# Performance work log

Hardware: AMD Instinct MI355X
Metric: run time of the kernel (lower is better)

## Reference

```python
import jax, jax.numpy as jnp
import numpy as np

B, S, V = 2, 2048, 50257
MIN_TOKENS_RATIO = 0.25
WARMUP_STEPS = 1000
THRESHOLD_SENSITIVITY = 0.5


def setup_inputs() -> dict:
    key = jax.random.key(0)
    k1, k2 = jax.random.split(key)
    logits = jax.random.normal(k1, (B, S, V), dtype=jnp.float32)
    targets = jax.random.randint(k2, (B, S), 0, V, dtype=jnp.int64)
    return {"logits": logits, "targets": targets, "step_count": 1000}


def _forward(logits, targets, step_count):
    vocab = logits.shape[-1]
    lf = logits.reshape(-1, vocab)          # (N, V)
    tf = targets.reshape(-1)                # (N,)
    n_tokens = lf.shape[0]

    # Single fused log-softmax pass shared by CE loss and difficulty scoring.
    logp = jax.nn.log_softmax(lf, axis=-1)  # (N, V)
    per_token_loss = -jnp.take_along_axis(logp, tf[:, None], axis=1)[:, 0]  # (N,)

    # --- difficulty scoring (no-grad in original: stop_gradient) ---
    logp_sg = jax.lax.stop_gradient(logp)
    p = jnp.exp(logp_sg)
    entropy = -jnp.sum(p * logp_sg, axis=-1)            # (N,)
    log_v = jnp.log(jnp.asarray(vocab, jnp.float32))
    ent_norm = entropy / log_v
    top2, _ = jax.lax.top_k(p, 2)                        # (N, 2)
    confidence = top2[:, 0]
    margin = top2[:, 0] - top2[:, 1]
    loss_norm = jax.lax.stop_gradient(per_token_loss) / log_v
    # 'combined' scoring: mean of normalized entropy, (1-margin), normalized loss
    difficulty = (ent_norm + (1.0 - margin) + loss_norm) / 3.0

    # --- warmup schedule + dynamic threshold ---
    progress = jnp.minimum(1.0, jnp.asarray(step_count, jnp.float32) / max(1, WARMUP_STEPS))
    base_ratio = 1.0 - progress * (1.0 - MIN_TOKENS_RATIO)
    mean_conf = jnp.mean(confidence)
    ratio = jnp.clip(base_ratio * (1.0 + THRESHOLD_SENSITIVITY * (0.5 - mean_conf)), 0.05, 1.0)

    # --- top-k selection via threshold on sorted difficulty (jit-safe dynamic k) ---
    k = jnp.clip(jnp.round(ratio * n_tokens).astype(jnp.int32), 1, n_tokens)
    sorted_desc = jnp.sort(difficulty)[::-1]
    thresh = jnp.take(sorted_desc, k - 1)
    mask = (difficulty >= thresh).astype(per_token_loss.dtype)  # (N,)

    tokens_selected = jnp.sum(mask)
    loss = jnp.sum(per_token_loss * mask) / jnp.maximum(tokens_selected, 1.0)
    return loss


def reference(logits, targets, step_count):
    return _forward(logits, targets, step_count)
```

## Files before the change

kernel.cpp:

```cpp
#include <hip/hip_runtime.h>

#define VOCAB 50257
#define NTOK 4096
#define P1_THREADS 256
#define P2_THREADS 1024
#define NEG_HUGE -3.402823466e+38f

struct OS { float m1, m2, Z, S1; };

__device__ __forceinline__ void os_init(OS& s) {
  s.m1 = NEG_HUGE; s.m2 = NEG_HUGE; s.Z = 0.0f; s.S1 = 0.0f;
}

__device__ __forceinline__ void os_update(OS& s, float x) {
  float nm1 = fmaxf(s.m1, x);
  float d   = s.m1 - nm1;
  float dx  = x - nm1;
  float ed  = __expf(d);
  float edx = __expf(dx);
  s.m2 = fmaxf(s.m2, fminf(s.m1, x));
  s.S1 = fmaf(dx, edx, ed * fmaf(d, s.Z, s.S1));
  s.Z  = fmaf(ed, s.Z, edx);
  s.m1 = nm1;
}

__device__ __forceinline__ void os_merge(OS& a, const OS& b) {
  float M   = fmaxf(a.m1, b.m1);
  float m2  = fmaxf(fmaxf(a.m2, b.m2), fminf(a.m1, b.m1));
  float ea  = __expf(a.m1 - M);
  float eb  = __expf(b.m1 - M);
  float S1  = ea * fmaf(a.m1 - M, a.Z, a.S1) + eb * fmaf(b.m1 - M, b.Z, b.S1);
  float Z   = fmaf(ea, a.Z, eb * b.Z);
  a.m1 = M; a.m2 = m2; a.Z = Z; a.S1 = S1;
}

__global__ __launch_bounds__(P1_THREADS) void cggr_rowstats(
    const float* __restrict__ logits, const int* __restrict__ targets,
    float* __restrict__ diff, float* __restrict__ loss, float* __restrict__ conf)
{
  const int row = blockIdx.x;
  const float* __restrict__ x = logits + (size_t)row * VOCAB;
  const int tid = threadIdx.x;

  float xt = 0.0f;
  if (tid == 0) {
    int t = targets[row];
    xt = x[t];
  }

  OS s0, s1, s2, s3;
  os_init(s0); os_init(s1); os_init(s2); os_init(s3);

  const int head = (4 - (row & 3)) & 3;
  const int nv4  = (VOCAB - head) >> 2;
  const float4* __restrict__ x4 = (const float4*)(x + head);

  for (int i = tid; i < nv4; i += P1_THREADS) {
    float4 v = x4[i];
    os_update(s0, v.x);
    os_update(s1, v.y);
    os_update(s2, v.z);
    os_update(s3, v.w);
  }
  if (tid < head) os_update(s0, x[tid]);
  for (int i = head + 4 * nv4 + tid; i < VOCAB; i += P1_THREADS) os_update(s1, x[i]);

  os_merge(s0, s1); os_merge(s2, s3); os_merge(s0, s2);

  for (int m = 1; m < 64; m <<= 1) {
    OS o;
    o.m1 = __shfl_xor(s0.m1, m);
    o.m2 = __shfl_xor(s0.m2, m);
    o.Z  = __shfl_xor(s0.Z,  m);
    o.S1 = __shfl_xor(s0.S1, m);
    os_merge(s0, o);
  }

  __shared__ OS sred[P1_THREADS / 64];
  const int lane = tid & 63, wid = tid >> 6;
  if (lane == 0) sred[wid] = s0;
  __syncthreads();

  if (tid == 0) {
    OS a = sred[0];
    for (int w = 1; w < P1_THREADS / 64; ++w) os_merge(a, sred[w]);
    float m       = a.m1;
    float lnZ     = logf(a.Z);
    float ptl     = m + lnZ - xt;
    float entropy = lnZ - a.S1 / a.Z;
    float log_v   = logf((float)VOCAB);
    float cf      = 1.0f / a.Z;
    float margin  = (1.0f - __expf(a.m2 - m)) / a.Z;
    float dif     = (entropy / log_v + (1.0f - margin) + ptl / log_v) / 3.0f;
    diff[row] = dif;
    loss[row] = ptl;
    conf[row] = cf;
  }
}

__global__ __launch_bounds__(P2_THREADS) void cggr_finalize(
    const float* __restrict__ diff, const float* __restrict__ loss,
    const float* __restrict__ conf, const int* __restrict__ step_ptr,
    float* __restrict__ out)
{
  __shared__ float s[NTOK];
  __shared__ float rl[P2_THREADS / 64];
  __shared__ float rc[P2_THREADS / 64];
  __shared__ int ks;

  const int tid  = threadIdx.x;
  const int lane = tid & 63, wid = tid >> 6;

  float c = 0.0f;
  for (int i = tid; i < NTOK; i += P2_THREADS) c += conf[i];
  for (int m = 1; m < 64; m <<= 1) c += __shfl_xor(c, m);
  if (lane == 0) rl[wid] = c;
  __syncthreads();

  if (tid == 0) {
    float sum = 0.0f;
    for (int w = 0; w < P2_THREADS / 64; ++w) sum += rl[w];
    float mean_conf  = sum / (float)NTOK;
    float step       = (float)step_ptr[0];
    float progress   = fminf(1.0f, step / 1000.0f);
    float base_ratio = 1.0f - progress * (1.0f - 0.25f);
    float ratio      = base_ratio * (1.0f + 0.5f * (0.5f - mean_conf));
    ratio = fminf(fmaxf(ratio, 0.05f), 1.0f);
    int k = (int)rintf(ratio * (float)NTOK);
    k = k < 1 ? 1 : (k > NTOK ? NTOK : k);
    ks = k;
  }

  for (int i = tid; i < NTOK; i += P2_THREADS) s[i] = diff[i];
  __syncthreads();

  for (int size = 2; size <= NTOK; size <<= 1) {
    for (int stride = size >> 1; stride > 0; stride >>= 1) {
      for (int t = tid; t < NTOK / 2; t += P2_THREADS) {
        int i = 2 * t - (t & (stride - 1));
        int j = i + stride;
        bool up = ((i & size) == 0);
        float a = s[i], b = s[j];
        if ((a > b) == up) { s[i] = b; s[j] = a; }
      }
      __syncthreads();
    }
  }

  const float thresh = s[NTOK - ks];

  float ls = 0.0f, cnt = 0.0f;
  for (int i = tid; i < NTOK; i += P2_THREADS) {
    float d = diff[i];
    if (d >= thresh) { ls += loss[i]; cnt += 1.0f; }
  }
  for (int m = 1; m < 64; m <<= 1) {
    ls  += __shfl_xor(ls, m);
    cnt += __shfl_xor(cnt, m);
  }
  if (lane == 0) { rl[wid] = ls; rc[wid] = cnt; }
  __syncthreads();
  if (tid == 0) {
    float tl = 0.0f, tc = 0.0f;
    for (int w = 0; w < P2_THREADS / 64; ++w) { tl += rl[w]; tc += rc[w]; }
    out[0] = tl / fmaxf(tc, 1.0f);
  }
}

extern "C" void kernel_launch(void* const* d_in, const int* in_sizes, int n_in,
                              void* d_out, int out_size, void* d_ws, size_t ws_size,
                              hipStream_t stream) {
  const float* logits  = (const float*)d_in[0];
  const int*   targets = (const int*)d_in[1];
  const int*   step    = (const int*)d_in[2];
  float* ws   = (float*)d_ws;
  float* diff = ws;
  float* loss = ws + NTOK;
  float* conf = ws + 2 * NTOK;

  hipLaunchKernelGGL(cggr_rowstats, dim3(NTOK), dim3(P1_THREADS), 0, stream,
                     logits, targets, diff, loss, conf);
  hipLaunchKernelGGL(cggr_finalize, dim3(1), dim3(P2_THREADS), 0, stream,
                     diff, loss, conf, step, (float*)d_out);
}
```

Measured before the change: 188.3 us.

## Batch online-softmax updates per float4 and replace bitonic sort with radix select

The row-stats kernel now reduces each float4 locally (max, second max, four exps) and merges once into the running state. That cuts the per-element rescale exponentials from two to roughly one plus a quarter, and the merge uses a single exp via a select. The finalize kernel drops the full 4096-element bitonic sort in shared memory. It finds the k-th largest difficulty with a 32-step bitwise radix select on order-preserving integer keys, using wave-level counts and a double-buffered shared reduction. The second kernel is a single block, so this mainly shortens its serial tail, while the first kernel is limited by memory bandwidth.

```diff
diff --git a/kernel.cpp b/kernel.cpp
--- a/kernel.cpp
+++ b/kernel.cpp
@@ -6,32 +6,35 @@
 #define P2_THREADS 1024
 #define NEG_HUGE -3.402823466e+38f
 
-struct OS { float m1, m2, Z, S1; };
+struct OS { float m, m2, Z, S1; };
 
 __device__ __forceinline__ void os_init(OS& s) {
-  s.m1 = NEG_HUGE; s.m2 = NEG_HUGE; s.Z = 0.0f; s.S1 = 0.0f;
+  s.m = NEG_HUGE; s.m2 = NEG_HUGE; s.Z = 0.0f; s.S1 = 0.0f;
 }
 
-__device__ __forceinline__ void os_update(OS& s, float x) {
-  float nm1 = fmaxf(s.m1, x);
-  float d   = s.m1 - nm1;
-  float dx  = x - nm1;
-  float ed  = __expf(d);
-  float edx = __expf(dx);
-  s.m2 = fmaxf(s.m2, fminf(s.m1, x));
-  s.S1 = fmaf(dx, edx, ed * fmaf(d, s.Z, s.S1));
-  s.Z  = fmaf(ed, s.Z, edx);
-  s.m1 = nm1;
+__device__ __forceinline__ void os_merge(OS& a, float ml, float m2l, float zl, float s1l) {
+  float M  = fmaxf(a.m, ml);
+  float mn = fminf(a.m, ml);
+  float m2 = fmaxf(fmaxf(a.m2, m2l), mn);
+  float e  = __expf(mn - M);
+  bool  om = a.m >= ml;
+  float eo = om ? 1.0f : e;
+  float en = om ? e : 1.0f;
+  float S1 = eo * fmaf(a.m - M, a.Z, a.S1) + en * fmaf(ml - M, zl, s1l);
+  float Z  = fmaf(eo, a.Z, en * zl);
+  a.m = M; a.m2 = m2; a.Z = Z; a.S1 = S1;
 }
 
-__device__ __forceinline__ void os_merge(OS& a, const OS& b) {
-  float M   = fmaxf(a.m1, b.m1);
-  float m2  = fmaxf(fmaxf(a.m2, b.m2), fminf(a.m1, b.m1));
-  float ea  = __expf(a.m1 - M);
-  float eb  = __expf(b.m1 - M);
-  float S1  = ea * fmaf(a.m1 - M, a.Z, a.S1) + eb * fmaf(b.m1 - M, b.Z, b.S1);
-  float Z   = fmaf(ea, a.Z, eb * b.Z);
-  a.m1 = M; a.m2 = m2; a.Z = Z; a.S1 = S1;
+__device__ __forceinline__ void os_update4(OS& s, float4 v) {
+  float a  = fmaxf(v.x, v.y), b = fminf(v.x, v.y);
+  float c  = fmaxf(v.z, v.w), d = fminf(v.z, v.w);
+  float ml  = fmaxf(a, c);
+  float m2l = fmaxf(fminf(a, c), fmaxf(b, d));
+  float d0 = v.x - ml, d1 = v.y - ml, d2 = v.z - ml, d3 = v.w - ml;
+  float e0 = __expf(d0), e1 = __expf(d1), e2 = __expf(d2), e3 = __expf(d3);
+  float zl  = (e0 + e1) + (e2 + e3);
+  float s1l = fmaf(d0, e0, fmaf(d1, e1, fmaf(d2, e2, d3 * e3)));
+  os_merge(s, ml, m2l, zl, s1l);
 }
 
 __global__ __launch_bounds__(P1_THREADS) void cggr_rowstats(
@@ -43,37 +46,36 @@
   const int tid = threadIdx.x;
 
   float xt = 0.0f;
-  if (tid == 0) {
-    int t = targets[row];
-    xt = x[t];
-  }
-
-  OS s0, s1, s2, s3;
-  os_init(s0); os_init(s1); os_init(s2); os_init(s3);
+  if (tid == 0) xt = x[targets[row]];
 
   const int head = (4 - (row & 3)) & 3;
   const int nv4  = (VOCAB - head) >> 2;
   const float4* __restrict__ x4 = (const float4*)(x + head);
 
-  for (int i = tid; i < nv4; i += P1_THREADS) {
-    float4 v = x4[i];
-    os_update(s0, v.x);
-    os_update(s1, v.y);
-    os_update(s2, v.z);
-    os_update(s3, v.w);
+  OS s0, s1; os_init(s0); os_init(s1);
+
+  int i = tid;
+  for (; i + P1_THREADS < nv4; i += 2 * P1_THREADS) {
+    float4 va = x4[i];
+    float4 vb = x4[i + P1_THREADS];
+    os_update4(s0, va);
+    os_update4(s1, vb);
   }
-  if (tid < head) os_update(s0, x[tid]);
-  for (int i = head + 4 * nv4 + tid; i < VOCAB; i += P1_THREADS) os_update(s1, x[i]);
+  if (i < nv4) os_update4(s0, x4[i]);
 
-  os_merge(s0, s1); os_merge(s2, s3); os_merge(s0, s2);
+  if (tid < head) os_merge(s1, x[tid], NEG_HUGE, 1.0f, 0.0f);
+  for (int t = head + 4 * nv4 + tid; t < VOCAB; t += P1_THREADS)
+    os_merge(s1, x[t], NEG_HUGE, 1.0f, 0.0f);
+
+  os_merge(s0, s1.m, s1.m2, s1.Z, s1.S1);
 
   for (int m = 1; m < 64; m <<= 1) {
     OS o;
-    o.m1 = __shfl_xor(s0.m1, m);
+    o.m  = __shfl_xor(s0.m,  m);
     o.m2 = __shfl_xor(s0.m2, m);
     o.Z  = __shfl_xor(s0.Z,  m);
     o.S1 = __shfl_xor(s0.S1, m);
-    os_merge(s0, o);
+    os_merge(s0, o.m, o.m2, o.Z, o.S1);
   }
 
   __shared__ OS sred[P1_THREADS / 64];
@@ -83,8 +85,9 @@
 
   if (tid == 0) {
     OS a = sred[0];
-    for (int w = 1; w < P1_THREADS / 64; ++w) os_merge(a, sred[w]);
-    float m       = a.m1;
+    for (int w = 1; w < P1_THREADS / 64; ++w)
+      os_merge(a, sred[w].m, sred[w].m2, sred[w].Z, sred[w].S1);
+    float m       = a.m;
     float lnZ     = logf(a.Z);
     float ptl     = m + lnZ - xt;
     float entropy = lnZ - a.S1 / a.Z;
@@ -103,66 +106,71 @@
     const float* __restrict__ conf, const int* __restrict__ step_ptr,
     float* __restrict__ out)
 {
-  __shared__ float s[NTOK];
-  __shared__ float rl[P2_THREADS / 64];
-  __shared__ float rc[P2_THREADS / 64];
-  __shared__ int ks;
+  __shared__ float redF[16];
+  __shared__ int   redI[2][16];
+  __shared__ float redL[16], redC[16];
 
-  const int tid  = threadIdx.x;
-  const int lane = tid & 63, wid = tid >> 6;
+  const int tid = threadIdx.x, lane = tid & 63, wid = tid >> 6;
 
-  float c = 0.0f;
-  for (int i = tid; i < NTOK; i += P2_THREADS) c += conf[i];
-  for (int m = 1; m < 64; m <<= 1) c += __shfl_xor(c, m);
-  if (lane == 0) rl[wid] = c;
-  __syncthreads();
-
-  if (tid == 0) {
-    float sum = 0.0f;
-    for (int w = 0; w < P2_THREADS / 64; ++w) sum += rl[w];
-    float mean_conf  = sum / (float)NTOK;
-    float step       = (float)step_ptr[0];
-    float progress   = fminf(1.0f, step / 1000.0f);
-    float base_ratio = 1.0f - progress * (1.0f - 0.25f);
-    float ratio      = base_ratio * (1.0f + 0.5f * (0.5f - mean_conf));
-    ratio = fminf(fmaxf(ratio, 0.05f), 1.0f);
-    int k = (int)rintf(ratio * (float)NTOK);
-    k = k < 1 ? 1 : (k > NTOK ? NTOK : k);
-    ks = k;
+  float dv[4];
+  unsigned u[4];
+  float cs = 0.0f;
+  #pragma unroll
+  for (int j = 0; j < 4; ++j) {
+    int i = tid + P2_THREADS * j;
+    dv[j] = diff[i];
+    cs   += conf[i];
+    unsigned b = __float_as_uint(dv[j]);
+    u[j] = b ^ ((b & 0x80000000u) ? 0xFFFFFFFFu : 0x80000000u);
   }
 
-  for (int i = tid; i < NTOK; i += P2_THREADS) s[i] = diff[i];
+  for (int m = 1; m < 64; m <<= 1) cs += __shfl_xor(cs, m);
+  if (lane == 0) redF[wid] = cs;
   __syncthreads();
+  float sum = 0.0f;
+  #pragma unroll
+  for (int w = 0; w < 16; ++w) sum += redF[w];
+  float mean_conf  = sum / (float)NTOK;
+  float step       = (float)step_ptr[0];
+  float progress   = fminf(1.0f, step / 1000.0f);
+  float base_ratio = 1.0f - progress * (1.0f - 0.25f);
+  float ratio      = base_ratio * (1.0f + 0.5f * (0.5f - mean_conf));
+  ratio = fminf(fmaxf(ratio, 0.05f), 1.0f);
+  int k = (int)rintf(ratio * (float)NTOK);
+  k = k < 1 ? 1 : (k > NTOK ? NTOK : k);
 
-  for (int size = 2; size <= NTOK; size <<= 1) {
-    for (int stride = size >> 1; stride > 0; stride >>= 1) {
-      for (int t = tid; t < NTOK / 2; t += P2_THREADS) {
-        int i = 2 * t - (t & (stride - 1));
-        int j = i + stride;
-        bool up = ((i & size) == 0);
-        float a = s[i], b = s[j];
-        if ((a > b) == up) { s[i] = b; s[j] = a; }
-      }
-      __syncthreads();
-    }
+  unsigned T = 0;
+  int parity = 0;
+  for (int bit = 31; bit >= 0; --bit) {
+    unsigned cand = T | (1u << bit);
+    int cnt = (u[0] >= cand) + (u[1] >= cand) + (u[2] >= cand) + (u[3] >= cand);
+    for (int m = 1; m < 64; m <<= 1) cnt += __shfl_xor(cnt, m);
+    if (lane == 0) redI[parity][wid] = cnt;
+    __syncthreads();
+    int tot = 0;
+    #pragma unroll
+    for (int w = 0; w < 16; ++w) tot += redI[parity][w];
+    if (tot >= k) T = cand;
+    parity ^= 1;
   }
+  unsigned tb = (T & 0x80000000u) ? (T ^ 0x80000000u) : ~T;
+  float thresh = __uint_as_float(tb);
 
-  const float thresh = s[NTOK - ks];
-
-  float ls = 0.0f, cnt = 0.0f;
-  for (int i = tid; i < NTOK; i += P2_THREADS) {
-    float d = diff[i];
-    if (d >= thresh) { ls += loss[i]; cnt += 1.0f; }
+  float ls = 0.0f, cn = 0.0f;
+  #pragma unroll
+  for (int j = 0; j < 4; ++j) {
+    if (dv[j] >= thresh) { ls += loss[tid + P2_THREADS * j]; cn += 1.0f; }
   }
   for (int m = 1; m < 64; m <<= 1) {
-    ls  += __shfl_xor(ls, m);
-    cnt += __shfl_xor(cnt, m);
+    ls += __shfl_xor(ls, m);
+    cn += __shfl_xor(cn, m);
   }
-  if (lane == 0) { rl[wid] = ls; rc[wid] = cnt; }
+  if (lane == 0) { redL[wid] = ls; redC[wid] = cn; }
   __syncthreads();
   if (tid == 0) {
     float tl = 0.0f, tc = 0.0f;
-    for (int w = 0; w < P2_THREADS / 64; ++w) { tl += rl[w]; tc += rc[w]; }
+    #pragma unroll
+    for (int w = 0; w < 16; ++w) { tl += redL[w]; tc += redC[w]; }
     out[0] = tl / fmaxf(tc, 1.0f);
   }
 }
```

After: 172.8 us. 8.2% less time.
